# Kernel tuning notes

Hardware: AMD Instinct MI355X
Metric: run time of the kernel (lower is better)

Reference implementation:

```python
import jax, jax.numpy as jnp
import numpy as np

NUM_HEADS = 8
DIMS = 512
SR = 2
EPS = 1e-6


def setup_inputs() -> dict:
    key = jax.random.key(0)
    ks = jax.random.split(key, 12)
    B, H, W, C = 4, 64, 64, DIMS
    s = 0.02
    return {
        "x": jax.random.normal(ks[0], (B, H * W, C), dtype=jnp.float32),
        "Wq": jax.random.normal(ks[1], (C, DIMS), dtype=jnp.float32) * s,
        "bq": jnp.zeros((DIMS,), jnp.float32),
        "Wk": jax.random.normal(ks[2], (C, DIMS), dtype=jnp.float32) * s,
        "bk": jnp.zeros((DIMS,), jnp.float32),
        "Wv": jax.random.normal(ks[3], (C, DIMS), dtype=jnp.float32) * s,
        "bv": jnp.zeros((DIMS,), jnp.float32),
        "Wp": jax.random.normal(ks[4], (DIMS, DIMS), dtype=jnp.float32) * s,
        "bp": jnp.zeros((DIMS,), jnp.float32),
        "sr_w": jax.random.normal(ks[5], (SR, SR, C, DIMS), dtype=jnp.float32) * s,  # HWIO
        "sr_b": jnp.zeros((DIMS,), jnp.float32),
        "ln_g": jnp.ones((DIMS,), jnp.float32),
        "ln_b": jnp.zeros((DIMS,), jnp.float32),
        "H": 64,
        "W": 64,
    }


def reference(x, Wq, bq, Wk, bk, Wv, bv, Wp, bp, sr_w, sr_b, ln_g, ln_b, H, W):
    B, N, C = x.shape
    hd = DIMS // NUM_HEADS

    # spatial-reduction of K/V: strided conv (kernel=stride=SR, SAME) + LayerNorm
    kv = x.reshape(B, H, W, C)
    kv = jax.lax.conv_general_dilated(
        kv, sr_w, window_strides=(SR, SR), padding="SAME",
        dimension_numbers=("NHWC", "HWIO", "NHWC")) + sr_b
    kv = kv.reshape(B, -1, C)  # [B, Nk, C], Nk = (H//SR)*(W//SR)
    mu = jnp.mean(kv, axis=-1, keepdims=True)
    var = jnp.mean(jnp.square(kv - mu), axis=-1, keepdims=True)
    kv = (kv - mu) * jax.lax.rsqrt(var + EPS) * ln_g + ln_b
    Nk = kv.shape[1]

    # NOTE: original splits heads as reshape(B, N, head_dims, num_heads) and
    # indexes the LAST axis per head -> head h sees channels d*NUM_HEADS+h.
    q = (x @ Wq + bq).reshape(B, N, hd, NUM_HEADS)
    k = (kv @ Wk + bk).reshape(B, Nk, hd, NUM_HEADS)
    v = (kv @ Wv + bv).reshape(B, Nk, hd, NUM_HEADS)

    scores = jnp.einsum("bqdh,bkdh->bhqk", q, k) / jnp.sqrt(jnp.float32(hd))
    w = jax.nn.softmax(scores, axis=-1)
    # concat of heads along channels -> (B, N, NUM_HEADS, hd) layout
    out = jnp.einsum("bhqk,bkdh->bqhd", w, v).reshape(B, N, DIMS)
    return out @ Wp + bp
```

## Files before the change

kernel.cpp:

```cpp
#include <hip/hip_runtime.h>


typedef __attribute__((ext_vector_type(8))) _Float16 f16x8;
typedef __attribute__((ext_vector_type(4))) _Float16 f16x4;
typedef __attribute__((ext_vector_type(4))) float f32x4;

#define EXP2F(x) __builtin_amdgcn_exp2f(x)

__device__ __forceinline__ void gload_lds16(const _Float16* g, _Float16* l)
{
    __builtin_amdgcn_global_load_lds(
        (const __attribute__((address_space(1))) void*)g,
        (__attribute__((address_space(3))) void*)l, 16, 0, 0);
}

__global__ __launch_bounds__(256)
void prep_k(const float* __restrict__ x,
            const float* __restrict__ Wq, const float* __restrict__ Wk,
            const float* __restrict__ Wv, const float* __restrict__ Wp,
            const float* __restrict__ srw,
            _Float16* __restrict__ xh, _Float16* __restrict__ wqt,
            _Float16* __restrict__ wkvt, _Float16* __restrict__ wpt,
            _Float16* __restrict__ srwt)
{
    __shared__ float T[32][33];
    const int id = blockIdx.x;
    const int t = threadIdx.x;

    if (id < 4096) {
        const size_t i = ((size_t)id * 256 + t) * 8;
        const float4 a = *(const float4*)(x + i);
        const float4 b = *(const float4*)(x + i + 4);
        f16x8 o;
        o[0] = (_Float16)a.x; o[1] = (_Float16)a.y; o[2] = (_Float16)a.z; o[3] = (_Float16)a.w;
        o[4] = (_Float16)b.x; o[5] = (_Float16)b.y; o[6] = (_Float16)b.z; o[7] = (_Float16)b.w;
        *(f16x8*)(xh + i) = o;
        return;
    }

    if (id < 5120) {
        const int id2 = id - 4096;
        const int z = id2 >> 8, k0 = ((id2 >> 4) & 15) * 32, n0 = (id2 & 15) * 32;
        const float* src; _Float16* dst; int perm;
        switch (z) {
            case 0:  src = Wq; dst = wqt;           perm = 1; break;
            case 1:  src = Wk; dst = wkvt;          perm = 1; break;
            case 2:  src = Wv; dst = wkvt + 262144; perm = 0; break;
            default: src = Wp; dst = wpt;           perm = 0; break;
        }
        {
            const int r = t >> 3, c = (t & 7) * 4;
            const float4 v = *(const float4*)(src + (size_t)(k0 + r) * 512 + n0 + c);
            T[r][c + 0] = v.x; T[r][c + 1] = v.y; T[r][c + 2] = v.z; T[r][c + 3] = v.w;
        }
        __syncthreads();
        {
            const int j = t >> 3, i0 = (t & 7) * 4;
            const int n = n0 + j;
            const int nper = perm ? ((n & 7) * 64 + (n >> 3)) : n;
            f16x4 o;
            o[0] = (_Float16)T[i0 + 0][j];
            o[1] = (_Float16)T[i0 + 1][j];
            o[2] = (_Float16)T[i0 + 2][j];
            o[3] = (_Float16)T[i0 + 3][j];
            *(f16x4*)(dst + (size_t)nper * 512 + k0 + i0) = o;
        }
        return;
    }

    {
        const int id3 = id - 5120;
        const int n0 = (id3 & 15) * 32, k0 = (id3 >> 4) * 32;
        {
            const int r = t >> 3, c = (t & 7) * 4;
            const float4 v = *(const float4*)(srw + (size_t)(k0 + r) * 512 + n0 + c);
            T[r][c + 0] = v.x; T[r][c + 1] = v.y; T[r][c + 2] = v.z; T[r][c + 3] = v.w;
        }
        __syncthreads();
        {
            const int j = t >> 3, i0 = (t & 7) * 4;
            f16x4 o;
            o[0] = (_Float16)T[i0 + 0][j];
            o[1] = (_Float16)T[i0 + 1][j];
            o[2] = (_Float16)T[i0 + 2][j];
            o[3] = (_Float16)T[i0 + 3][j];
            *(f16x4*)(srwt + (size_t)(n0 + j) * 2048 + k0 + i0) = o;
        }
        return;
    }
}

template<int MODE, bool CONV, int BM>
__device__ __forceinline__ void gemm_body(
    const int bx, const int by,
    const _Float16* __restrict__ A, const _Float16* __restrict__ Wt,
    const float* __restrict__ bias, const float* __restrict__ bias2,
    void* __restrict__ Cv, void* __restrict__ Cv2,
    _Float16* __restrict__ As, _Float16* __restrict__ Ws)
{
    constexpr int K = CONV ? 2048 : 512;
    constexpr int NIT = K / 32;
    constexpr int MT = BM / 32;
    constexpr int AI = BM / 64;
    constexpr int ABUF = BM * 32;
    const int tid = threadIdx.x;
    const int wave = tid >> 6, lane = tid & 63;
    const int quad = lane >> 4, l15 = lane & 15;
    const int wm = wave >> 1, wn = wave & 1;
    const int wrow = wm * (BM / 2);
    const int m0 = by * BM, n0 = bx * 128;

    f32x4 acc[MT][4] = {};

    auto stage = [&](const int k0, const int buf) {
        #pragma unroll
        for (int t = 0; t < AI; ++t) {
            const int ii = wave * AI + t;
            const int e = ii * 64 + lane;
            const int row = e >> 2, c8 = (e & 3) * 8;
            const _Float16* gp;
            if (CONV) {
                const int grow = m0 + row;
                const int b = grow >> 10, rem = grow & 1023;
                const int oh = rem >> 5, ow = rem & 31;
                const int gk = k0 + c8;
                const int ky = (gk >> 10) & 1, kx = (gk >> 9) & 1, ci = gk & 511;
                gp = A + ((size_t)((b * 64 + 2 * oh + ky) * 64) + (2 * ow + kx)) * 512 + ci;
            } else {
                gp = A + (size_t)(m0 + row) * K + k0 + c8;
            }
            gload_lds16(gp, &As[buf * ABUF + ii * 512]);
        }
        #pragma unroll
        for (int t = 0; t < 2; ++t) {
            const int ii = wave * 2 + t;
            const int e = ii * 64 + lane;
            const int row = e >> 2, c8 = (e & 3) * 8;
            gload_lds16(Wt + (size_t)(n0 + row) * K + k0 + c8,
                        &Ws[buf * 4096 + ii * 512]);
        }
    };

    stage(0, 0);
    asm volatile("s_waitcnt vmcnt(0)" ::: "memory");
    __builtin_amdgcn_s_barrier();

    for (int it = 0; it < NIT; ++it) {
        const int cur = it & 1;
        if (it + 1 < NIT) stage((it + 1) * 32, cur ^ 1);

        f16x8 af[MT], bf[4];
        #pragma unroll
        for (int mt = 0; mt < MT; ++mt)
            af[mt] = *(const f16x8*)&As[cur * ABUF + (wrow + mt * 16 + l15) * 32 + quad * 8];
        #pragma unroll
        for (int nt = 0; nt < 4; ++nt)
            bf[nt] = *(const f16x8*)&Ws[cur * 4096 + (wn * 64 + nt * 16 + l15) * 32 + quad * 8];
        #pragma unroll
        for (int mt = 0; mt < MT; ++mt)
            #pragma unroll
            for (int nt = 0; nt < 4; ++nt)
                acc[mt][nt] = __builtin_amdgcn_mfma_f32_16x16x32_f16(
                    af[mt], bf[nt], acc[mt][nt], 0, 0, 0);

        asm volatile("s_waitcnt vmcnt(0)" ::: "memory");
        __builtin_amdgcn_s_barrier();
    }

    #pragma unroll
    for (int nt = 0; nt < 4; ++nt) {
        const int gcol = n0 + wn * 64 + nt * 16 + l15;
        float bv;
        if (MODE == 6) bv = bias[(gcol & 63) * 8 + (gcol >> 6)];
        else if (MODE == 5) bv = (gcol < 512) ? bias[(gcol & 63) * 8 + (gcol >> 6)]
                                              : bias2[gcol - 512];
        else bv = bias[gcol];
        #pragma unroll
        for (int mt = 0; mt < MT; ++mt) {
            const int row0 = m0 + wrow + mt * 16 + quad * 4;
            if (MODE == 0) {
                #pragma unroll
                for (int r = 0; r < 4; ++r)
                    ((float*)Cv)[(size_t)(row0 + r) * 512 + gcol] = acc[mt][nt][r] + bv;
            } else if (MODE == 4 || MODE == 6) {
                #pragma unroll
                for (int r = 0; r < 4; ++r)
                    ((_Float16*)Cv)[(size_t)(row0 + r) * 512 + gcol] =
                        (_Float16)(acc[mt][nt][r] + bv);
            } else {
                if (gcol < 512) {
                    #pragma unroll
                    for (int r = 0; r < 4; ++r)
                        ((_Float16*)Cv)[(size_t)(row0 + r) * 512 + gcol] =
                            (_Float16)(acc[mt][nt][r] + bv);
                } else {
                    const int c = gcol - 512;
                    const int h = c & 7, d = c >> 3;
                    const int b_ = row0 >> 10, jj = row0 & 1023;
                    f16x4 o;
                    #pragma unroll
                    for (int r = 0; r < 4; ++r) o[r] = (_Float16)(acc[mt][nt][r] + bv);
                    *(f16x4*)((_Float16*)Cv2 +
                              ((size_t)(b_ * 8 + h) * 64 + d) * 1024 + jj) = o;
                }
            }
        }
    }
}

template<int MODE, bool CONV, int BM>
__global__ __launch_bounds__(256)
void gemm_f16(const _Float16* __restrict__ A, const _Float16* __restrict__ Wt,
              const float* __restrict__ bias, const float* __restrict__ bias2,
              void* __restrict__ Cv, void* __restrict__ Cv2)
{
    __shared__ __align__(16) _Float16 As[2 * BM * 32];
    __shared__ __align__(16) _Float16 Ws[2 * 128 * 32];
    gemm_body<MODE, CONV, BM>(blockIdx.x, blockIdx.y, A, Wt, bias, bias2,
                              Cv, Cv2, As, Ws);
}

__global__ __launch_bounds__(256)
void convq_k(const _Float16* __restrict__ xh, const _Float16* __restrict__ srwt,
             const float* __restrict__ srb, const _Float16* __restrict__ wqt,
             const float* __restrict__ bq,
             _Float16* __restrict__ kvh, _Float16* __restrict__ qh)
{
    __shared__ __align__(16) _Float16 As[2 * 128 * 32];
    __shared__ __align__(16) _Float16 Ws[2 * 128 * 32];
    const int id = blockIdx.x;
    if (id < 256) {
        gemm_body<4, true, 64>(id & 3, id >> 2, xh, srwt, srb, nullptr,
                               kvh, nullptr, As, Ws);
    } else {
        const int id2 = id - 256;
        gemm_body<6, false, 128>(id2 & 3, id2 >> 2, xh, wqt, bq, nullptr,
                                 qh, nullptr, As, Ws);
    }
}

__global__ __launch_bounds__(256)
void ln_k(_Float16* __restrict__ buf, const float* __restrict__ g,
          const float* __restrict__ b)
{
    const int row = blockIdx.x;
    _Float16* p = buf + (size_t)row * 512;
    const int tid = threadIdx.x;
    const float vx = (float)p[tid * 2], vy = (float)p[tid * 2 + 1];
    float s = vx + vy, q = vx * vx + vy * vy;
    #pragma unroll
    for (int off = 32; off > 0; off >>= 1) {
        s += __shfl_xor(s, off);
        q += __shfl_xor(q, off);
    }
    __shared__ float ss[4], sq[4], stat[2];
    const int wid = tid >> 6;
    if ((tid & 63) == 0) { ss[wid] = s; sq[wid] = q; }
    __syncthreads();
    if (tid == 0) {
        const float S = ss[0] + ss[1] + ss[2] + ss[3];
        const float Q = sq[0] + sq[1] + sq[2] + sq[3];
        const float mu = S * (1.f / 512.f);
        const float var = fmaxf(Q * (1.f / 512.f) - mu * mu, 0.f);
        stat[0] = mu;
        stat[1] = rsqrtf(var + 1e-6f);
    }
    __syncthreads();
    const float mu = stat[0], rs = stat[1];
    const float2 gg = *(const float2*)(g + tid * 2);
    const float2 bb = *(const float2*)(b + tid * 2);
    p[tid * 2]     = (_Float16)((vx - mu) * rs * gg.x + bb.x);
    p[tid * 2 + 1] = (_Float16)((vy - mu) * rs * gg.y + bb.y);
}

__global__ __launch_bounds__(512)
void attn_mfma_k(const _Float16* __restrict__ qb,
                 const _Float16* __restrict__ kbuf,
                 const _Float16* __restrict__ vbuf,
                 _Float16* __restrict__ out)
{
    const int bh = blockIdx.y;
    const int qt = blockIdx.x;
    const int b = bh >> 3, h = bh & 7;
    const int tid = threadIdx.x;
    const int wave = tid >> 6, lane = tid & 63;
    const int quad = lane >> 4, l15 = lane & 15;

    __shared__ __align__(16) _Float16 Ks[2][64 * 72];
    __shared__ __align__(16) _Float16 Vs[2][64 * 72];

    const int qrow = b * 4096 + qt * 512 + wave * 64 + l15;
    const _Float16* qp = qb + (size_t)qrow * 512 + h * 64 + quad * 8;
    f16x8 qf[4][2];
    #pragma unroll
    for (int su = 0; su < 4; ++su) {
        qf[su][0] = *(const f16x8*)(qp + su * 16 * 512);
        qf[su][1] = *(const f16x8*)(qp + su * 16 * 512 + 32);
    }
    {
        const _Float16 qs = (_Float16)0.18033688f;
        #pragma unroll
        for (int su = 0; su < 4; ++su)
            #pragma unroll
            for (int g = 0; g < 2; ++g)
                #pragma unroll
                for (int i = 0; i < 8; ++i) qf[su][g][i] *= qs;
    }

    const int kr = tid >> 3, kc = (tid & 7) * 8;
    const int krp = (kr & 32) | ((kr & 4) << 2) | ((kr >> 1) & 12) | (kr & 3);
    const _Float16* kg = kbuf + (size_t)(b * 1024 + kr) * 512 + h * 64 + kc;
    const _Float16* vg = vbuf + (size_t)(bh * 64 + kr) * 1024 + kc;

    f16x8 krg = *(const f16x8*)kg;
    f16x8 vrg = *(const f16x8*)vg;
    *(f16x8*)&Ks[0][krp * 72 + kc] = krg;
    *(f16x8*)&Vs[0][kr * 72 + kc] = vrg;

    float l_run[4] = {0.f, 0.f, 0.f, 0.f};
    f32x4 acc[4][4] = {};

    for (int kt = 0; kt < 16; ++kt) {
        const int cur = kt & 1;
        __syncthreads();
        if (kt < 15) {
            krg = *(const f16x8*)(kg + (size_t)(kt + 1) * 64 * 512);
            vrg = *(const f16x8*)(vg + (kt + 1) * 64);
        }

        #pragma unroll
        for (int kb = 0; kb < 2; ++kb) {
            f16x8 pa[4];
            #pragma unroll
            for (int c = 0; c < 2; ++c) {
                const int ct = kb * 2 + c;
                const f16x8 kf0 = *(const f16x8*)&Ks[cur][(ct * 16 + l15) * 72 + quad * 8];
                const f16x8 kf1 = *(const f16x8*)&Ks[cur][(ct * 16 + l15) * 72 + 32 + quad * 8];
                #pragma unroll
                for (int su = 0; su < 4; ++su) {
                    f32x4 s = {};
                    s = __builtin_amdgcn_mfma_f32_16x16x32_f16(kf0, qf[su][0], s, 0, 0, 0);
                    s = __builtin_amdgcn_mfma_f32_16x16x32_f16(kf1, qf[su][1], s, 0, 0, 0);
                    const float p0 = EXP2F(s[0]), p1 = EXP2F(s[1]);
                    const float p2 = EXP2F(s[2]), p3 = EXP2F(s[3]);
                    l_run[su] += (p0 + p1) + (p2 + p3);
                    pa[su][c * 4 + 0] = (_Float16)p0;
                    pa[su][c * 4 + 1] = (_Float16)p1;
                    pa[su][c * 4 + 2] = (_Float16)p2;
                    pa[su][c * 4 + 3] = (_Float16)p3;
                }
            }
            __builtin_amdgcn_s_setprio(1);
            #pragma unroll
            for (int nt = 0; nt < 4; ++nt) {
                const f16x8 vf = *(const f16x8*)&Vs[cur][(nt * 16 + l15) * 72 + kb * 32 + quad * 8];
                #pragma unroll
                for (int su = 0; su < 4; ++su)
                    acc[su][nt] = __builtin_amdgcn_mfma_f32_16x16x32_f16(
                        pa[su], vf, acc[su][nt], 0, 0, 0);
            }
            __builtin_amdgcn_s_setprio(0);
        }

        if (kt < 15) {
            *(f16x8*)&Ks[cur ^ 1][krp * 72 + kc] = krg;
            *(f16x8*)&Vs[cur ^ 1][kr * 72 + kc] = vrg;
        }
    }

    #pragma unroll
    for (int su = 0; su < 4; ++su) {
        float ts = l_run[su];
        ts += __shfl_xor(ts, 16);
        ts += __shfl_xor(ts, 32);
        float inv[4];
        #pragma unroll
        for (int r = 0; r < 4; ++r)
            inv[r] = 1.0f / __shfl(ts, quad * 4 + r, 16);
        #pragma unroll
        for (int nt = 0; nt < 4; ++nt)
            #pragma unroll
            for (int r = 0; r < 4; ++r) {
                const int row = qt * 512 + wave * 64 + su * 16 + quad * 4 + r;
                const int col = h * 64 + nt * 16 + l15;
                out[((size_t)b * 4096 + row) * 512 + col] =
                    (_Float16)(acc[su][nt][r] * inv[r]);
            }
    }
}

extern "C" void kernel_launch(void* const* d_in, const int* in_sizes, int n_in,
                              void* d_out, int out_size, void* d_ws, size_t ws_size,
                              hipStream_t stream)
{
    const float* x   = (const float*)d_in[0];
    const float* Wq  = (const float*)d_in[1];
    const float* bq  = (const float*)d_in[2];
    const float* Wk  = (const float*)d_in[3];
    const float* bk  = (const float*)d_in[4];
    const float* Wv  = (const float*)d_in[5];
    const float* bv  = (const float*)d_in[6];
    const float* Wp  = (const float*)d_in[7];
    const float* bp  = (const float*)d_in[8];
    const float* srw = (const float*)d_in[9];
    const float* srb = (const float*)d_in[10];
    const float* lng = (const float*)d_in[11];
    const float* lnb = (const float*)d_in[12];

    _Float16* ws   = (_Float16*)d_ws;
    _Float16* xh   = ws;
    _Float16* atth = xh + 8388608;
    _Float16* kvh  = atth + 8388608;
    _Float16* kh   = kvh + 2097152;
    _Float16* vh   = kh + 2097152;
    _Float16* wqt  = vh + 2097152;
    _Float16* wkvt = wqt + 262144;
    _Float16* wpt  = wkvt + 524288;
    _Float16* srwt = wpt + 262144;
    _Float16* qh   = (_Float16*)d_out;

    prep_k<<<6144, 256, 0, stream>>>(x, Wq, Wk, Wv, Wp, srw,
                                     xh, wqt, wkvt, wpt, srwt);
    convq_k<<<768, 256, 0, stream>>>(xh, srwt, srb, wqt, bq, kvh, qh);
    ln_k<<<4096, 256, 0, stream>>>(kvh, lng, lnb);
    gemm_f16<5, false, 64><<<dim3(8, 64), 256, 0, stream>>>(
        kvh, wkvt, bk, bv, kh, vh);
    attn_mfma_k<<<dim3(8, 32), 512, 0, stream>>>(qh, kh, vh, atth);
    gemm_f16<0, false, 128><<<dim3(4, 128), 256, 0, stream>>>(
        atth, wpt, bp, nullptr, d_out, nullptr);
}
```

Measured before the change: 227.9 us.

## Deepen GEMM LDS pipeline to 3-4 stages with partial vmcnt waits

Replaces the double-buffered GEMM mainloop with a multi-stage ring buffer: three stages for BM=128 and four for BM=64. Each iteration waits only on the oldest outstanding load group using counted vmcnt, then barriers once, so several tiles of global-to-LDS loads stay in flight during the MFMA work. It also precomputes per-thread base addresses so the staging loop does less address math. LDS use per block rises to 48KB, which can lower occupancy, and the per-stage vmcnt constants have to match the number of loads issued per stage.

```diff
diff --git a/kernel.cpp b/kernel.cpp
--- a/kernel.cpp
+++ b/kernel.cpp
@@ -12,6 +12,12 @@
     __builtin_amdgcn_global_load_lds(
         (const __attribute__((address_space(1))) void*)g,
         (__attribute__((address_space(3))) void*)l, 16, 0, 0);
+}
+
+template<int N>
+__device__ __forceinline__ void wait_vm()
+{
+    asm volatile("s_waitcnt vmcnt(%0)" :: "n"(N) : "memory");
 }
 
 __global__ __launch_bounds__(256)
@@ -103,6 +109,9 @@
     constexpr int MT = BM / 32;
     constexpr int AI = BM / 64;
     constexpr int ABUF = BM * 32;
+    constexpr int NBUF = (BM == 64) ? 4 : 3;
+    constexpr int P = NBUF - 1;
+    constexpr int L = AI + 2;
     const int tid = threadIdx.x;
     const int wave = tid >> 6, lane = tid & 63;
     const int quad = lane >> 4, l15 = lane & 15;
@@ -110,44 +119,69 @@
     const int wrow = wm * (BM / 2);
     const int m0 = by * BM, n0 = bx * 128;
 
-    f32x4 acc[MT][4] = {};
+    const _Float16* abase[AI];
+    int ac8[AI];
+    #pragma unroll
+    for (int t = 0; t < AI; ++t) {
+        const int e = (wave * AI + t) * 64 + lane;
+        const int row = e >> 2, c8 = (e & 3) * 8;
+        ac8[t] = c8;
+        if (CONV) {
+            const int grow = m0 + row;
+            const int b = grow >> 10, rem = grow & 1023;
+            const int oh = rem >> 5, ow = rem & 31;
+            abase[t] = A + ((size_t)((b * 64 + 2 * oh) * 64) + 2 * ow) * 512;
+        } else {
+            abase[t] = A + (size_t)(m0 + row) * K + c8;
+        }
+    }
+    const _Float16* wbase[2];
+    #pragma unroll
+    for (int t = 0; t < 2; ++t) {
+        const int e = (wave * 2 + t) * 64 + lane;
+        const int row = e >> 2, c8 = (e & 3) * 8;
+        wbase[t] = Wt + (size_t)(n0 + row) * K + c8;
+    }
 
     auto stage = [&](const int k0, const int buf) {
         #pragma unroll
         for (int t = 0; t < AI; ++t) {
-            const int ii = wave * AI + t;
-            const int e = ii * 64 + lane;
-            const int row = e >> 2, c8 = (e & 3) * 8;
             const _Float16* gp;
             if (CONV) {
-                const int grow = m0 + row;
-                const int b = grow >> 10, rem = grow & 1023;
-                const int oh = rem >> 5, ow = rem & 31;
-                const int gk = k0 + c8;
-                const int ky = (gk >> 10) & 1, kx = (gk >> 9) & 1, ci = gk & 511;
-                gp = A + ((size_t)((b * 64 + 2 * oh + ky) * 64) + (2 * ow + kx)) * 512 + ci;
+                const int gk = k0 + ac8[t];
+                gp = abase[t] + ((gk >> 10) & 1) * 32768 + ((gk >> 9) & 1) * 512
+                              + (gk & 511);
             } else {
-                gp = A + (size_t)(m0 + row) * K + k0 + c8;
+                gp = abase[t] + k0;
             }
-            gload_lds16(gp, &As[buf * ABUF + ii * 512]);
-        }
-        #pragma unroll
-        for (int t = 0; t < 2; ++t) {
-            const int ii = wave * 2 + t;
-            const int e = ii * 64 + lane;
-            const int row = e >> 2, c8 = (e & 3) * 8;
-            gload_lds16(Wt + (size_t)(n0 + row) * K + k0 + c8,
-                        &Ws[buf * 4096 + ii * 512]);
-        }
+            gload_lds16(gp, &As[buf * ABUF + (wave * AI + t) * 512]);
+        }
+        #pragma unroll
+        for (int t = 0; t < 2; ++t)
+            gload_lds16(wbase[t] + k0, &Ws[buf * 4096 + (wave * 2 + t) * 512]);
     };
 
-    stage(0, 0);
-    asm volatile("s_waitcnt vmcnt(0)" ::: "memory");
-    __builtin_amdgcn_s_barrier();
-
+    f32x4 acc[MT][4] = {};
+
+    #pragma unroll
+    for (int p = 0; p < P; ++p) stage(p * 32, p);
+
+    int cur = 0, nxt = P % NBUF;
     for (int it = 0; it < NIT; ++it) {
-        const int cur = it & 1;
-        if (it + 1 < NIT) stage((it + 1) * 32, cur ^ 1);
+        int rem = NIT - 1 - it;
+        if (rem > P - 1) rem = P - 1;
+        switch (rem) {
+            case 0:  wait_vm<0>(); break;
+            case 1:  wait_vm<L>(); break;
+            case 2:  wait_vm<2 * L>(); break;
+            default: wait_vm<3 * L>(); break;
+        }
+        __builtin_amdgcn_s_barrier();
+        __builtin_amdgcn_sched_barrier(0);
+        if (it + P < NIT) {
+            stage((it + P) * 32, nxt);
+            nxt = (nxt + 1 == NBUF) ? 0 : nxt + 1;
+        }
 
         f16x8 af[MT], bf[4];
         #pragma unroll
@@ -163,8 +197,7 @@
                 acc[mt][nt] = __builtin_amdgcn_mfma_f32_16x16x32_f16(
                     af[mt], bf[nt], acc[mt][nt], 0, 0, 0);
 
-        asm volatile("s_waitcnt vmcnt(0)" ::: "memory");
-        __builtin_amdgcn_s_barrier();
+        cur = (cur + 1 == NBUF) ? 0 : cur + 1;
     }
 
     #pragma unroll
@@ -214,10 +247,10 @@
               const float* __restrict__ bias, const float* __restrict__ bias2,
               void* __restrict__ Cv, void* __restrict__ Cv2)
 {
-    __shared__ __align__(16) _Float16 As[2 * BM * 32];
-    __shared__ __align__(16) _Float16 Ws[2 * 128 * 32];
+    __shared__ __align__(16) _Float16 lds[24576];
+    constexpr int NBUF = (BM == 64) ? 4 : 3;
     gemm_body<MODE, CONV, BM>(blockIdx.x, blockIdx.y, A, Wt, bias, bias2,
-                              Cv, Cv2, As, Ws);
+                              Cv, Cv2, lds, lds + NBUF * BM * 32);
 }
 
 __global__ __launch_bounds__(256)
@@ -226,16 +259,15 @@
              const float* __restrict__ bq,
              _Float16* __restrict__ kvh, _Float16* __restrict__ qh)
 {
-    __shared__ __align__(16) _Float16 As[2 * 128 * 32];
-    __shared__ __align__(16) _Float16 Ws[2 * 128 * 32];
+    __shared__ __align__(16) _Float16 lds[24576];
     const int id = blockIdx.x;
     if (id < 256) {
         gemm_body<4, true, 64>(id & 3, id >> 2, xh, srwt, srb, nullptr,
-                               kvh, nullptr, As, Ws);
+                               kvh, nullptr, lds, lds + 4 * 64 * 32);
     } else {
         const int id2 = id - 256;
         gemm_body<6, false, 128>(id2 & 3, id2 >> 2, xh, wqt, bq, nullptr,
-                                 qh, nullptr, As, Ws);
+                                 qh, nullptr, lds, lds + 3 * 128 * 32);
     }
 }
 
```

Measured after the change: 209.7 us. 8.0% less time.
